# Performance work log

Measured on AMD Instinct MI355X. Metric: run time of the kernel, lower is better.

## Reference

```python
import jax, jax.numpy as jnp
import numpy as np
from jax import lax

B, T, D, H = 64, 2048, 256, 256


def setup_inputs() -> dict:
    key = jax.random.key(0)
    k1, k2, k3 = jax.random.split(key, 3)
    xs = jax.random.normal(k1, (B, T, D), dtype=jnp.float32)
    # scale weights ~ 1/sqrt(fan_in) to keep tanh out of saturation
    W_ih = jax.random.normal(k2, (D, H), dtype=jnp.float32) / np.sqrt(D)
    W_hh = jax.random.normal(k3, (H, H), dtype=jnp.float32) / np.sqrt(H)
    b_hh = jnp.zeros((H,), dtype=jnp.float32)
    c = jnp.zeros((B, H), dtype=jnp.float32)
    return {"c": c, "xs": xs, "W_ih": W_ih, "W_hh": W_hh, "b_hh": b_hh}


def reference(c, xs, W_ih, W_hh, b_hh):
    # Elman RNN: h_t = tanh(x_t @ W_ih + h_{t-1} @ W_hh + b_hh)
    # (the ih bias is created but never applied in the original module)
    # Precompute the input projection for all timesteps in one big GEMM.
    px = jnp.einsum('btd,dh->bth', xs, W_ih)  # [B, T, H]

    def step(h, px_t):
        h_new = jnp.tanh(h @ W_hh + b_hh + px_t)
        return h_new, h_new

    h_final, ys = lax.scan(step, c, px.transpose(1, 0, 2))  # ys: [T, B, H]
    return h_final, ys.transpose(1, 0, 2)  # carry [B,H], outputs [B,T,H]
```

## Files before the change

kernel.cpp:

```cpp
#include <hip/hip_runtime.h>


typedef _Float16 half8 __attribute__((ext_vector_type(8)));
typedef float floatx4 __attribute__((ext_vector_type(4)));
typedef float f32x4 __attribute__((ext_vector_type(4)));

constexpr int Bb = 64, Tt = 2048, Dd = 256, Hh = 256;

__device__ __forceinline__ int lds_addr(int row, int col) {
    return row * 512 + ((((col >> 3) ^ (row & 7)) & 31) << 4) + ((col & 7) << 1);
}

__device__ __forceinline__ float fast_tanh(float x) {
    float e = __builtin_amdgcn_exp2f(x * 2.885390081777927f);
    float r = __builtin_amdgcn_rcpf(e + 1.0f);
    return __builtin_fmaf(-2.0f, r, 1.0f);
}

__device__ __forceinline__ __amdgpu_buffer_rsrc_t mkrsrc(void* p, unsigned bytes) {
    return __builtin_amdgcn_make_buffer_rsrc(p, (short)0, (int)bytes, 0x00020000);
}

__device__ __forceinline__ float buf_load_f32(__amdgpu_buffer_rsrc_t rs, int voff, int soff) {
    union { int i; float f; } u;
    u.i = __builtin_amdgcn_raw_buffer_load_b32(rs, voff, soff, 0);
    return u.f;
}

__device__ __forceinline__ void buf_store_f32(float v, __amdgpu_buffer_rsrc_t rs, int voff, int soff) {
    union { float f; int i; } u;
    u.f = v;
    __builtin_amdgcn_raw_buffer_store_b32(u.i, rs, voff, soff, 0);
}

#define LDS_BARRIER() asm volatile("s_waitcnt lgkmcnt(0)\n\ts_barrier" ::: "memory")

__global__ __launch_bounds__(256, 2) void px_gemm(const float* __restrict__ xs,
                                                  const float* __restrict__ Wih,
                                                  const float* __restrict__ bhh,
                                                  float* __restrict__ px) {
    const int lane = threadIdx.x & 63;
    const int w = threadIdx.x >> 6;
    const int q = lane >> 4;
    const int m = lane & 15;

    half8 bf[4][8];
#pragma unroll
    for (int tt = 0; tt < 4; ++tt) {
        const int n = 64 * w + 16 * tt + m;
#pragma unroll
        for (int c = 0; c < 8; ++c) {
            half8 f;
#pragma unroll
            for (int j = 0; j < 8; ++j)
                f[j] = (_Float16)Wih[(32 * c + 8 * q + j) * Hh + n];
            bf[tt][c] = f;
        }
    }
    float bias[4];
#pragma unroll
    for (int tt = 0; tt < 4; ++tt) bias[tt] = bhh[64 * w + 16 * tt + m];

    for (int i = 0; i < 8; ++i) {
        const int tau = blockIdx.x * 8 + i;
        const float* arow = xs + (size_t)(tau * 16 + m) * Dd;
        half8 af[8];
#pragma unroll
        for (int c = 0; c < 8; ++c) {
            f32x4 lo = *(const f32x4*)(arow + 32 * c + 8 * q);
            f32x4 hi = *(const f32x4*)(arow + 32 * c + 8 * q + 4);
            half8 f;
            f[0] = (_Float16)lo[0]; f[1] = (_Float16)lo[1];
            f[2] = (_Float16)lo[2]; f[3] = (_Float16)lo[3];
            f[4] = (_Float16)hi[0]; f[5] = (_Float16)hi[1];
            f[6] = (_Float16)hi[2]; f[7] = (_Float16)hi[3];
            af[c] = f;
        }
        floatx4 acc[4];
#pragma unroll
        for (int tt = 0; tt < 4; ++tt) {
            acc[tt][0] = bias[tt]; acc[tt][1] = bias[tt];
            acc[tt][2] = bias[tt]; acc[tt][3] = bias[tt];
        }
#pragma unroll
        for (int c = 0; c < 8; ++c)
#pragma unroll
            for (int tt = 0; tt < 4; ++tt)
                acc[tt] = __builtin_amdgcn_mfma_f32_16x16x32_f16(af[c], bf[tt][c], acc[tt], 0, 0, 0);
#pragma unroll
        for (int tt = 0; tt < 4; ++tt)
#pragma unroll
            for (int r = 0; r < 4; ++r)
                px[(size_t)(tau * 16 + 4 * q + r) * Hh + 64 * w + 16 * tt + m] = acc[tt][r];
    }
}

__global__ __launch_bounds__(512, 2) void rnn_scan(const float* __restrict__ c0,
                                                   const float* __restrict__ Whh,
                                                   float* __restrict__ hfin,
                                                   float* __restrict__ ys) {
    __shared__ alignas(16) unsigned char hb[2][8192];
    const int g = blockIdx.x;
    const int lane = threadIdx.x & 63;
    const int w = threadIdx.x >> 6;
    const int q = lane >> 4;
    const int m = lane & 15;

    const __amdgpu_buffer_rsrc_t rsYS = mkrsrc(ys, (unsigned)Bb * Tt * Hh * 4u);
    const __amdgpu_buffer_rsrc_t rsHF = mkrsrc(hfin, (unsigned)Bb * Hh * 4u);

    half8 bf[2][8];
#pragma unroll
    for (int tt = 0; tt < 2; ++tt) {
        const int n = 32 * w + 16 * tt + m;
#pragma unroll
        for (int c = 0; c < 8; ++c) {
            half8 f;
#pragma unroll
            for (int j = 0; j < 8; ++j)
                f[j] = (_Float16)Whh[(32 * c + 8 * q + j) * Hh + n];
            bf[tt][c] = f;
        }
    }

    for (int i = threadIdx.x; i < 16 * 256; i += 512) {
        const int row = i >> 8, col = i & 255;
        *(_Float16*)&hb[0][lds_addr(row, col)] = (_Float16)c0[(16 * g + row) * Hh + col];
    }

    int boff[8];
#pragma unroll
    for (int tt = 0; tt < 2; ++tt)
#pragma unroll
        for (int r = 0; r < 4; ++r)
            boff[4 * tt + r] =
                (int)(((16 * g + 4 * q + r) * Tt) * Hh + 32 * w + 16 * tt + m) * 4;

    int ard[8];
#pragma unroll
    for (int c = 0; c < 8; ++c)
        ard[c] = m * 512 + ((((4 * c + q) ^ (m & 7)) & 31) << 4);

    int wad[8];
#pragma unroll
    for (int tt = 0; tt < 2; ++tt)
#pragma unroll
        for (int r = 0; r < 4; ++r)
            wad[4 * tt + r] = lds_addr(4 * q + r, 32 * w + 16 * tt + m);

    floatx4 pxA[2], pxB[2];
#pragma unroll
    for (int k = 0; k < 8; ++k)
        pxA[k >> 2][k & 3] = buf_load_f32(rsYS, boff[k], 0);

    __syncthreads();

#define RNN_STEP(P, PXC, PXN, LASTCHK, TCUR)                                   \
    {                                                                          \
                                 \
        half8 af[8];                                                           \
        _Pragma("unroll") for (int c2 = 0; c2 < 8; ++c2)                       \
            af[c2] = *(const half8*)&hb[(P)][ard[c2]];                         \
                       \
        const int soffN = ((TCUR) + 1) << 10;                                  \
        _Pragma("unroll") for (int k2 = 0; k2 < 8; ++k2)                       \
            PXN[k2 >> 2][k2 & 3] = buf_load_f32(rsYS, boff[k2], soffN);        \
        floatx4 acc0 = PXC[0], acc1 = PXC[1];                                  \
        _Pragma("unroll") for (int c2 = 0; c2 < 8; ++c2)                       \
            acc0 = __builtin_amdgcn_mfma_f32_16x16x32_f16(af[c2], bf[0][c2],   \
                                                          acc0, 0, 0, 0);      \
        _Pragma("unroll") for (int c2 = 0; c2 < 8; ++c2)                       \
            acc1 = __builtin_amdgcn_mfma_f32_16x16x32_f16(af[c2], bf[1][c2],   \
                                                          acc1, 0, 0, 0);      \
        const int soffC = (TCUR) << 10;                                        \
        _Pragma("unroll") for (int r2 = 0; r2 < 4; ++r2) {                     \
            const float hv = fast_tanh(acc0[r2]);                              \
            buf_store_f32(hv, rsYS, boff[r2], soffC);                          \
            *(_Float16*)&hb[(P) ^ 1][wad[r2]] = (_Float16)hv;                  \
            if ((LASTCHK) && (TCUR) == Tt - 1)                                 \
                buf_store_f32(hv, rsHF,                                        \
                    ((16 * g + 4 * q + r2) * Hh + 32 * w + m) * 4, 0);         \
        }                                                                      \
        _Pragma("unroll") for (int r2 = 0; r2 < 4; ++r2) {                     \
            const float hv = fast_tanh(acc1[r2]);                              \
            buf_store_f32(hv, rsYS, boff[4 + r2], soffC);                      \
            *(_Float16*)&hb[(P) ^ 1][wad[4 + r2]] = (_Float16)hv;              \
            if ((LASTCHK) && (TCUR) == Tt - 1)                                 \
                buf_store_f32(hv, rsHF,                                        \
                    ((16 * g + 4 * q + r2) * Hh + 32 * w + 16 + m) * 4, 0);    \
        }                                                                      \
        LDS_BARRIER();                                                         \
    }

    for (int t = 0; t < Tt; t += 2) {
        RNN_STEP(0, pxA, pxB, 0, t)
        RNN_STEP(1, pxB, pxA, 1, t + 1)
    }
#undef RNN_STEP
}

extern "C" void kernel_launch(void* const* d_in, const int* in_sizes, int n_in,
                              void* d_out, int out_size, void* d_ws, size_t ws_size,
                              hipStream_t stream) {
    const float* c0  = (const float*)d_in[0];
    const float* xs  = (const float*)d_in[1];
    const float* Wih = (const float*)d_in[2];
    const float* Whh = (const float*)d_in[3];
    const float* bhh = (const float*)d_in[4];
    float* out = (float*)d_out;
    float* hfin = out;
    float* ys = out + Bb * Hh;

    px_gemm<<<1024, 256, 0, stream>>>(xs, Wih, bhh, ys);
    rnn_scan<<<Bb / 16, 512, 0, stream>>>(c0, Whh, hfin, ys);
}
```

Baseline: 1.845 ms.

## Swap MFMA operands to transpose accumulators and vectorize px/ys accesses

Swaps the A and B operands of the MFMA in both the input-projection GEMM and the recurrent scan, so each lane's accumulator holds four consecutive hidden units of one batch row instead of four batch rows of one unit. This lets px/ys loads and stores use 128-bit buffer operations and the LDS hidden-state writes use 64-bit half4 stores, replacing many scalar accesses per step. The bias is now loaded as a vector matching the new layout. It aims to cut memory instruction count on the latency-bound serial scan, at the cost of a different LDS write pattern that may change bank conflicts.

Result: slower. 2.263 ms (+22.7%).

```diff
diff --git a/kernel.cpp b/kernel.cpp
--- a/kernel.cpp
+++ b/kernel.cpp
@@ -2,8 +2,10 @@
 
 
 typedef _Float16 half8 __attribute__((ext_vector_type(8)));
+typedef _Float16 half4 __attribute__((ext_vector_type(4)));
 typedef float floatx4 __attribute__((ext_vector_type(4)));
 typedef float f32x4 __attribute__((ext_vector_type(4)));
+typedef int int4v __attribute__((ext_vector_type(4)));
 
 constexpr int Bb = 64, Tt = 2048, Dd = 256, Hh = 256;
 
@@ -21,16 +23,13 @@
     return __builtin_amdgcn_make_buffer_rsrc(p, (short)0, (int)bytes, 0x00020000);
 }
 
-__device__ __forceinline__ float buf_load_f32(__amdgpu_buffer_rsrc_t rs, int voff, int soff) {
-    union { int i; float f; } u;
-    u.i = __builtin_amdgcn_raw_buffer_load_b32(rs, voff, soff, 0);
-    return u.f;
-}
-
-__device__ __forceinline__ void buf_store_f32(float v, __amdgpu_buffer_rsrc_t rs, int voff, int soff) {
-    union { float f; int i; } u;
-    u.f = v;
-    __builtin_amdgcn_raw_buffer_store_b32(u.i, rs, voff, soff, 0);
+__device__ __forceinline__ floatx4 buf_load_f32x4(__amdgpu_buffer_rsrc_t rs, int voff, int soff) {
+    int4v v = __builtin_amdgcn_raw_buffer_load_b128(rs, voff, soff, 0);
+    return __builtin_bit_cast(floatx4, v);
+}
+
+__device__ __forceinline__ void buf_store_f32x4(floatx4 v, __amdgpu_buffer_rsrc_t rs, int voff, int soff) {
+    __builtin_amdgcn_raw_buffer_store_b128(__builtin_bit_cast(int4v, v), rs, voff, soff, 0);
 }
 
 #define LDS_BARRIER() asm volatile("s_waitcnt lgkmcnt(0)\n\ts_barrier" ::: "memory")
@@ -57,9 +56,10 @@
             bf[tt][c] = f;
         }
     }
-    float bias[4];
-#pragma unroll
-    for (int tt = 0; tt < 4; ++tt) bias[tt] = bhh[64 * w + 16 * tt + m];
+    f32x4 bias2[4];
+#pragma unroll
+    for (int tt = 0; tt < 4; ++tt)
+        bias2[tt] = *(const f32x4*)(bhh + 64 * w + 16 * tt + 4 * q);
 
     for (int i = 0; i < 8; ++i) {
         const int tau = blockIdx.x * 8 + i;
@@ -79,19 +79,18 @@
         floatx4 acc[4];
 #pragma unroll
         for (int tt = 0; tt < 4; ++tt) {
-            acc[tt][0] = bias[tt]; acc[tt][1] = bias[tt];
-            acc[tt][2] = bias[tt]; acc[tt][3] = bias[tt];
+            acc[tt][0] = bias2[tt][0]; acc[tt][1] = bias2[tt][1];
+            acc[tt][2] = bias2[tt][2]; acc[tt][3] = bias2[tt][3];
         }
 #pragma unroll
         for (int c = 0; c < 8; ++c)
 #pragma unroll
             for (int tt = 0; tt < 4; ++tt)
-                acc[tt] = __builtin_amdgcn_mfma_f32_16x16x32_f16(af[c], bf[tt][c], acc[tt], 0, 0, 0);
+                acc[tt] = __builtin_amdgcn_mfma_f32_16x16x32_f16(bf[tt][c], af[c], acc[tt], 0, 0, 0);
 #pragma unroll
         for (int tt = 0; tt < 4; ++tt)
-#pragma unroll
-            for (int r = 0; r < 4; ++r)
-                px[(size_t)(tau * 16 + 4 * q + r) * Hh + 64 * w + 16 * tt + m] = acc[tt][r];
+            *(f32x4*)(px + (size_t)(tau * 16 + m) * Hh + 64 * w + 16 * tt + 4 * q) =
+                *(f32x4*)&acc[tt];
     }
 }
 
@@ -128,30 +127,24 @@
         *(_Float16*)&hb[0][lds_addr(row, col)] = (_Float16)c0[(16 * g + row) * Hh + col];
     }
 
-    int boff[8];
+    int voff[2];
 #pragma unroll
     for (int tt = 0; tt < 2; ++tt)
-#pragma unroll
-        for (int r = 0; r < 4; ++r)
-            boff[4 * tt + r] =
-                (int)(((16 * g + 4 * q + r) * Tt) * Hh + 32 * w + 16 * tt + m) * 4;
+        voff[tt] = (((16 * g + m) * Tt) * Hh + 32 * w + 16 * tt + 4 * q) * 4;
 
     int ard[8];
 #pragma unroll
     for (int c = 0; c < 8; ++c)
         ard[c] = m * 512 + ((((4 * c + q) ^ (m & 7)) & 31) << 4);
 
-    int wad[8];
+    int wadp[2];
 #pragma unroll
     for (int tt = 0; tt < 2; ++tt)
-#pragma unroll
-        for (int r = 0; r < 4; ++r)
-            wad[4 * tt + r] = lds_addr(4 * q + r, 32 * w + 16 * tt + m);
+        wadp[tt] = lds_addr(m, 32 * w + 16 * tt + 4 * q);
 
     floatx4 pxA[2], pxB[2];
 #pragma unroll
-    for (int k = 0; k < 8; ++k)
-        pxA[k >> 2][k & 3] = buf_load_f32(rsYS, boff[k], 0);
+    for (int tt = 0; tt < 2; ++tt) pxA[tt] = buf_load_f32x4(rsYS, voff[tt], 0);
 
     __syncthreads();
 
@@ -161,33 +154,32 @@
         half8 af[8];                                                           \
         _Pragma("unroll") for (int c2 = 0; c2 < 8; ++c2)                       \
             af[c2] = *(const half8*)&hb[(P)][ard[c2]];                         \
-                       \
+                                 \
         const int soffN = ((TCUR) + 1) << 10;                                  \
-        _Pragma("unroll") for (int k2 = 0; k2 < 8; ++k2)                       \
-            PXN[k2 >> 2][k2 & 3] = buf_load_f32(rsYS, boff[k2], soffN);        \
+        PXN[0] = buf_load_f32x4(rsYS, voff[0], soffN);                         \
+        PXN[1] = buf_load_f32x4(rsYS, voff[1], soffN);                         \
         floatx4 acc0 = PXC[0], acc1 = PXC[1];                                  \
+           \
         _Pragma("unroll") for (int c2 = 0; c2 < 8; ++c2)                       \
-            acc0 = __builtin_amdgcn_mfma_f32_16x16x32_f16(af[c2], bf[0][c2],   \
+            acc0 = __builtin_amdgcn_mfma_f32_16x16x32_f16(bf[0][c2], af[c2],   \
                                                           acc0, 0, 0, 0);      \
         _Pragma("unroll") for (int c2 = 0; c2 < 8; ++c2)                       \
-            acc1 = __builtin_amdgcn_mfma_f32_16x16x32_f16(af[c2], bf[1][c2],   \
+            acc1 = __builtin_amdgcn_mfma_f32_16x16x32_f16(bf[1][c2], af[c2],   \
                                                           acc1, 0, 0, 0);      \
         const int soffC = (TCUR) << 10;                                        \
-        _Pragma("unroll") for (int r2 = 0; r2 < 4; ++r2) {                     \
-            const float hv = fast_tanh(acc0[r2]);                              \
-            buf_store_f32(hv, rsYS, boff[r2], soffC);                          \
-            *(_Float16*)&hb[(P) ^ 1][wad[r2]] = (_Float16)hv;                  \
+        _Pragma("unroll") for (int u2 = 0; u2 < 2; ++u2) {                     \
+            const floatx4 a2 = (u2 == 0) ? acc0 : acc1;                        \
+            floatx4 hv;                                                        \
+            _Pragma("unroll") for (int r2 = 0; r2 < 4; ++r2)                   \
+                hv[r2] = fast_tanh(a2[r2]);                                    \
+            buf_store_f32x4(hv, rsYS, voff[u2], soffC);                        \
+            half4 hp;                                                          \
+            _Pragma("unroll") for (int r2 = 0; r2 < 4; ++r2)                   \
+                hp[r2] = (_Float16)hv[r2];                                     \
+            *(half4*)&hb[(P) ^ 1][wadp[u2]] = hp;                              \
             if ((LASTCHK) && (TCUR) == Tt - 1)                                 \
-                buf_store_f32(hv, rsHF,                                        \
-                    ((16 * g + 4 * q + r2) * Hh + 32 * w + m) * 4, 0);         \
-        }                                                                      \
-        _Pragma("unroll") for (int r2 = 0; r2 < 4; ++r2) {                     \
-            const float hv = fast_tanh(acc1[r2]);                              \
-            buf_store_f32(hv, rsYS, boff[4 + r2], soffC);                      \
-            *(_Float16*)&hb[(P) ^ 1][wad[4 + r2]] = (_Float16)hv;              \
-            if ((LASTCHK) && (TCUR) == Tt - 1)                                 \
-                buf_store_f32(hv, rsHF,                                        \
-                    ((16 * g + 4 * q + r2) * Hh + 32 * w + 16 + m) * 4, 0);    \
+                buf_store_f32x4(hv, rsHF,                                      \
+                    ((16 * g + m) * Hh + 32 * w + 16 * u2 + 4 * q) * 4, 0);    \
         }                                                                      \
         LDS_BARRIER();                                                         \
     }
```
